# Performance work log

Hardware: AMD Instinct MI355X
Metric: run time of the kernel (lower is better)

## Reference

```python
import jax, jax.numpy as jnp
import numpy as np

N = 10000
E = 320000
DIN = 256
HID = 64
HEADS = 4
LAT = 32
NEG_SLOPE = 0.2


def _layer_params(key, din, heads, out_c):
    ks = jax.random.split(key, 6)
    s_in = 1.0 / np.sqrt(din)
    return dict(
        Wl=jax.random.normal(ks[0], (din, heads * out_c), jnp.float32) * s_in,
        bl=jnp.zeros((heads * out_c,), jnp.float32),
        Wr=jax.random.normal(ks[1], (din, heads * out_c), jnp.float32) * s_in,
        br=jnp.zeros((heads * out_c,), jnp.float32),
        att=jax.random.normal(ks[2], (heads, out_c), jnp.float32) * (1.0 / np.sqrt(out_c)),
        bo=jnp.zeros((heads * out_c,), jnp.float32),
    )


def setup_inputs() -> dict:
    key = jax.random.key(0)
    ks = jax.random.split(key, 8)
    inp = {
        "x": jax.random.normal(ks[0], (N, DIN), jnp.float32),
        "edge_index": jax.random.randint(ks[1], (2, E), 0, N, jnp.int64 if jax.config.jax_enable_x64 else jnp.int32),
        "eps": jax.random.normal(ks[2], (N, LAT), jnp.float32),
    }
    p0 = _layer_params(ks[3], DIN, HEADS, HID)
    p1 = _layer_params(ks[4], HID * HEADS, HEADS, HID)
    pmu = _layer_params(ks[5], HID * HEADS, 1, LAT)
    plv = _layer_params(ks[6], HID * HEADS, 1, LAT)
    for tag, p in (("l0", p0), ("l1", p1), ("mu", pmu), ("lv", plv)):
        for k, v in p.items():
            inp[f"{k}_{tag}"] = v
    return inp


def _gatv2(h, src, dst, Wl, bl, Wr, br, att, bo, heads, out_c, concat):
    # GATv2: e_ij = att . LeakyReLU(lin_l(x_j) + lin_r(x_i)), softmax over j for each i,
    # out_i = sum_j alpha_ij * lin_l(x_j). src = j (source), dst = i (target).
    xl = (h @ Wl + bl).reshape(-1, heads, out_c)  # [N,H,C]
    xr = (h @ Wr + br).reshape(-1, heads, out_c)
    e = jax.nn.leaky_relu(xl[src] + xr[dst], NEG_SLOPE)  # [E,H,C]
    score = jnp.einsum('ehc,hc->eh', e, att)             # [E,H]
    smax = jax.ops.segment_max(score, dst, num_segments=N)
    ex = jnp.exp(score - smax[dst])
    denom = jax.ops.segment_sum(ex, dst, num_segments=N)
    alpha = ex / (denom[dst] + 1e-16)                    # [E,H]
    out = jax.ops.segment_sum(alpha[:, :, None] * xl[src], dst, num_segments=N)  # [N,H,C]
    out = out.reshape(N, heads * out_c) if concat else out.mean(axis=1)
    return out + bo


def reference(x, edge_index, eps,
              Wl_l0, bl_l0, Wr_l0, br_l0, att_l0, bo_l0,
              Wl_l1, bl_l1, Wr_l1, br_l1, att_l1, bo_l1,
              Wl_mu, bl_mu, Wr_mu, br_mu, att_mu, bo_mu,
              Wl_lv, bl_lv, Wr_lv, br_lv, att_lv, bo_lv):
    loop = jnp.arange(N, dtype=edge_index.dtype)
    src = jnp.concatenate([edge_index[0], loop])  # add self-loops (PyG default)
    dst = jnp.concatenate([edge_index[1], loop])
    h = jax.nn.elu(_gatv2(x, src, dst, Wl_l0, bl_l0, Wr_l0, br_l0, att_l0, bo_l0, HEADS, HID, True))
    h = jax.nn.elu(_gatv2(h, src, dst, Wl_l1, bl_l1, Wr_l1, br_l1, att_l1, bo_l1, HEADS, HID, True))
    mu = _gatv2(h, src, dst, Wl_mu, bl_mu, Wr_mu, br_mu, att_mu, bo_mu, 1, LAT, False)
    log_var = _gatv2(h, src, dst, Wl_lv, bl_lv, Wr_lv, br_lv, att_lv, bo_lv, 1, LAT, False)
    z = mu + eps * jnp.exp(0.5 * log_var)  # reparameterize (training mode)
    adj_recon = z @ z.T                    # [N,N] dense decode
    return (adj_recon, mu, log_var)
```

## Files before the change

### kernel.cpp

```cpp
#include <hip/hip_runtime.h>
#include <hip/hip_bf16.h>
#include <math.h>

constexpr int Nn  = 10000;
constexpr int Ed  = 320000;
constexpr int DIN = 256;
constexpr float NEG = 0.2f;

constexpr size_t OFF_XL  = 0;
constexpr size_t OFF_XR  = 2560000;
constexpr size_t OFF_H   = 5120000;
constexpr size_t OFF_XSL = 7680000;
constexpr size_t OFF_XSR = 8320000;
constexpr size_t OFF_WLC = 8960000;
constexpr size_t OFF_WRC = 8976384;
constexpr size_t OFF_BLC = 8992768;
constexpr size_t OFF_BRC = 8992832;
constexpr size_t OFF_ATT = 8992896;
constexpr size_t OFF_BOC = 8992960;
constexpr size_t OFF_INT = 9000000;
constexpr int I_DEG = 0;
constexpr int I_ROW = 16384;
constexpr int I_CUR = 32768;
constexpr int I_CSR = 49152;
static_assert(OFF_INT + (I_CSR + Ed + Nn + 4) / 1 < 100000000, "scratch fits in adj region");

__global__ void k_init_deg(int* deg, int n) {
    int i = blockIdx.x * blockDim.x + threadIdx.x;
    if (i < n) deg[i] = 1;
}

__global__ void k_count(const int* __restrict__ dst, int* deg, int e) {
    int i = blockIdx.x * blockDim.x + threadIdx.x;
    if (i < e) atomicAdd(&deg[dst[i]], 1);
}

__global__ void k_scan(const int* __restrict__ deg, int* row_ptr, int* cursor, int n) {
    __shared__ int sums[256];
    int t = threadIdx.x;
    int chunk = (n + 255) / 256;
    int start = t * chunk, end = min(start + chunk, n);
    int s = 0;
    for (int i = start; i < end; ++i) s += deg[i];
    sums[t] = s;
    __syncthreads();
    for (int off = 1; off < 256; off <<= 1) {
        int v = (t >= off) ? sums[t - off] : 0;
        __syncthreads();
        sums[t] += v;
        __syncthreads();
    }
    int run = sums[t] - s;
    for (int i = start; i < end; ++i) { row_ptr[i] = run; cursor[i] = run; run += deg[i]; }
    if (t == 255) row_ptr[n] = sums[255];
}

__global__ void k_scatter(const int* __restrict__ src, const int* __restrict__ dst,
                          int* cursor, int* csr, int e, int n) {
    int i = blockIdx.x * blockDim.x + threadIdx.x;
    if (i < e) {
        int d = dst[i];
        int pos = atomicAdd(&cursor[d], 1);
        csr[pos] = src[i];
    } else if (i < e + n) {
        int v = i - e;
        int pos = atomicAdd(&cursor[v], 1);
        csr[pos] = v;
    }
}

__global__ __launch_bounds__(256) void k_gemm(const float* __restrict__ A,
                                              const float* __restrict__ W,
                                              const float* __restrict__ bias,
                                              float* __restrict__ out,
                                              int M, int Ncols) {
    constexpr int K = 256;
    __shared__ float As[32][68];
    __shared__ float Ws[32][64];
    int tid = threadIdx.x;
    int tx = tid & 15, ty = tid >> 4;
    int m0 = blockIdx.x * 64, n0 = blockIdx.y * 64;
    float acc[4][4] = {};
    int am = tid >> 2, akb = (tid & 3) * 8;
    int wk = tid >> 3, wnb = (tid & 7) * 8;
    const bool arow_ok = (m0 + am) < M;
    const float* Aptr = A + (size_t)(m0 + am) * K + akb;
    const float* Wptr = W + (size_t)wk * Ncols + n0 + wnb;

    for (int k0 = 0; k0 < K; k0 += 32) {
        float4 a0 = {0, 0, 0, 0}, a1 = {0, 0, 0, 0};
        if (arow_ok) {
            a0 = *(const float4*)(Aptr + k0);
            a1 = *(const float4*)(Aptr + k0 + 4);
        }
        float4 w0 = *(const float4*)(Wptr + (size_t)k0 * Ncols);
        float4 w1 = *(const float4*)(Wptr + (size_t)k0 * Ncols + 4);
        __syncthreads();
        As[akb + 0][am] = a0.x; As[akb + 1][am] = a0.y; As[akb + 2][am] = a0.z; As[akb + 3][am] = a0.w;
        As[akb + 4][am] = a1.x; As[akb + 5][am] = a1.y; As[akb + 6][am] = a1.z; As[akb + 7][am] = a1.w;
        *(float4*)&Ws[wk][wnb] = w0;
        *(float4*)&Ws[wk][wnb + 4] = w1;
        __syncthreads();
        #pragma unroll
        for (int k = 0; k < 32; ++k) {
            float4 a = *(const float4*)&As[k][ty * 4];
            float4 b = *(const float4*)&Ws[k][tx * 4];
            float av[4] = {a.x, a.y, a.z, a.w};
            float bv[4] = {b.x, b.y, b.z, b.w};
            #pragma unroll
            for (int i2 = 0; i2 < 4; ++i2)
                #pragma unroll
                for (int j2 = 0; j2 < 4; ++j2)
                    acc[i2][j2] = fmaf(av[i2], bv[j2], acc[i2][j2]);
        }
    }
    #pragma unroll
    for (int i2 = 0; i2 < 4; ++i2) {
        int row = m0 + ty * 4 + i2;
        if (row < M) {
            int col = n0 + tx * 4;
            float4 o;
            o.x = acc[i2][0] + bias[col + 0];
            o.y = acc[i2][1] + bias[col + 1];
            o.z = acc[i2][2] + bias[col + 2];
            o.w = acc[i2][3] + bias[col + 3];
            *(float4*)&out[(size_t)row * Ncols + col] = o;
        }
    }
}

__device__ __forceinline__ float lrelu(float x) { return x > 0.f ? x : NEG * x; }

template <bool DO_ELU>
__global__ __launch_bounds__(256) void k_gat4(const float* __restrict__ xl,
                                              const float* __restrict__ xr,
                                              const float* __restrict__ att,
                                              const float* __restrict__ bo,
                                              const int* __restrict__ row_ptr,
                                              const int* __restrict__ csr,
                                              float* __restrict__ out, int n) {
    int lane = threadIdx.x & 63;
    int node = (blockIdx.x * blockDim.x + threadIdx.x) >> 6;
    if (node >= n) return;
    int f = lane * 4;
    float4 xrr  = *(const float4*)&xr[(size_t)node * 256 + f];
    float4 attr = *(const float4*)&att[f];
    float m = -INFINITY, d = 0.f;
    float4 acc = {0.f, 0.f, 0.f, 0.f};

    int e0 = row_ptr[node], e1 = row_ptr[node + 1];
    int e = e0;
    for (; e + 1 < e1; e += 2) {
        int ja = csr[e], jb = csr[e + 1];
        float4 va = *(const float4*)&xl[(size_t)ja * 256 + f];
        float4 vb = *(const float4*)&xl[(size_t)jb * 256 + f];
        float ta = attr.x * lrelu(va.x + xrr.x) + attr.y * lrelu(va.y + xrr.y)
                 + attr.z * lrelu(va.z + xrr.z) + attr.w * lrelu(va.w + xrr.w);
        float tb = attr.x * lrelu(vb.x + xrr.x) + attr.y * lrelu(vb.y + xrr.y)
                 + attr.z * lrelu(vb.z + xrr.z) + attr.w * lrelu(vb.w + xrr.w);
        #pragma unroll
        for (int mask = 1; mask <= 8; mask <<= 1) {
            ta += __shfl_xor(ta, mask, 64);
            tb += __shfl_xor(tb, mask, 64);
        }
        float mn = fmaxf(m, fmaxf(ta, tb));
        float sc = __expf(m - mn);
        float pa = __expf(ta - mn), pb = __expf(tb - mn);
        d = d * sc + pa + pb;
        acc.x = acc.x * sc + pa * va.x + pb * vb.x;
        acc.y = acc.y * sc + pa * va.y + pb * vb.y;
        acc.z = acc.z * sc + pa * va.z + pb * vb.z;
        acc.w = acc.w * sc + pa * va.w + pb * vb.w;
        m = mn;
    }
    if (e < e1) {
        int j = csr[e];
        float4 v = *(const float4*)&xl[(size_t)j * 256 + f];
        float t = attr.x * lrelu(v.x + xrr.x) + attr.y * lrelu(v.y + xrr.y)
                + attr.z * lrelu(v.z + xrr.z) + attr.w * lrelu(v.w + xrr.w);
        #pragma unroll
        for (int mask = 1; mask <= 8; mask <<= 1) t += __shfl_xor(t, mask, 64);
        float mn = fmaxf(m, t);
        float sc = __expf(m - mn), p = __expf(t - mn);
        d = d * sc + p;
        acc.x = acc.x * sc + p * v.x;
        acc.y = acc.y * sc + p * v.y;
        acc.z = acc.z * sc + p * v.z;
        acc.w = acc.w * sc + p * v.w;
        m = mn;
    }
    float inv = 1.f / (d + 1e-16f);
    float4 bo4 = *(const float4*)&bo[f];
    float4 o;
    o.x = acc.x * inv + bo4.x;
    o.y = acc.y * inv + bo4.y;
    o.z = acc.z * inv + bo4.z;
    o.w = acc.w * inv + bo4.w;
    if (DO_ELU) {
        o.x = o.x > 0.f ? o.x : expm1f(o.x);
        o.y = o.y > 0.f ? o.y : expm1f(o.y);
        o.z = o.z > 0.f ? o.z : expm1f(o.z);
        o.w = o.w > 0.f ? o.w : expm1f(o.w);
    }
    *(float4*)&out[(size_t)node * 256 + f] = o;
}

template <int H, int C, bool DO_ELU, bool SPLIT>
__global__ __launch_bounds__(256) void k_gat(const float* __restrict__ xl,
                                             const float* __restrict__ xr,
                                             const float* __restrict__ att,
                                             const float* __restrict__ bo,
                                             const int* __restrict__ row_ptr,
                                             const int* __restrict__ csr,
                                             float* __restrict__ out0,
                                             float* __restrict__ out1, int n) {
    constexpr int F = H * C;
    constexpr int R = F / 64;
    int lane = threadIdx.x & 63;
    int node = (blockIdx.x * blockDim.x + threadIdx.x) >> 6;
    if (node >= n) return;

    float xrr[R], attr[R], m[R], d[R], acc[R];
    #pragma unroll
    for (int r = 0; r < R; ++r) {
        xrr[r]  = xr[(size_t)node * F + r * 64 + lane];
        attr[r] = att[r * 64 + lane];
        m[r] = -INFINITY;
        d[r] = 0.f;
        acc[r] = 0.f;
    }
    int e0 = row_ptr[node], e1 = row_ptr[node + 1];
    for (int e = e0; e < e1; ++e) {
        int j = csr[e];
        float v[R], s[R];
        #pragma unroll
        for (int r = 0; r < R; ++r) {
            v[r] = xl[(size_t)j * F + r * 64 + lane];
            float t = v[r] + xrr[r];
            t = (t > 0.f) ? t : NEG * t;
            t *= attr[r];
            #pragma unroll
            for (int mask = C / 2; mask >= 1; mask >>= 1)
                t += __shfl_xor(t, mask, 64);
            s[r] = t;
        }
        #pragma unroll
        for (int r = 0; r < R; ++r) {
            if (s[r] > m[r]) {
                float sc = __expf(m[r] - s[r]);
                d[r] *= sc; acc[r] *= sc; m[r] = s[r];
            }
            float p = __expf(s[r] - m[r]);
            d[r] += p;
            acc[r] = fmaf(p, v[r], acc[r]);
        }
    }
    #pragma unroll
    for (int r = 0; r < R; ++r) {
        float o = acc[r] / (d[r] + 1e-16f) + bo[r * 64 + lane];
        if (DO_ELU) o = (o > 0.f) ? o : expm1f(o);
        if (SPLIT) {
            int f = r * 64 + lane;
            int h = f / C, c = f % C;
            float* op = (h == 0) ? out0 : out1;
            op[(size_t)node * C + c] = o;
        } else {
            out0[(size_t)node * F + r * 64 + lane] = o;
        }
    }
}

__global__ void k_cat(const float* __restrict__ Wlmu, const float* __restrict__ Wllv,
                      const float* __restrict__ Wrmu, const float* __restrict__ Wrlv,
                      const float* __restrict__ blmu, const float* __restrict__ bllv,
                      const float* __restrict__ brmu, const float* __restrict__ brlv,
                      const float* __restrict__ attmu, const float* __restrict__ attlv,
                      const float* __restrict__ bomu, const float* __restrict__ bolv,
                      float* WLC, float* WRC, float* BLC, float* BRC, float* ATTC, float* BOC) {
    int i = blockIdx.x * blockDim.x + threadIdx.x;
    if (i < 256 * 64) {
        int k = i >> 6, c = i & 63;
        WLC[i] = (c < 32) ? Wlmu[k * 32 + c] : Wllv[k * 32 + c - 32];
        WRC[i] = (c < 32) ? Wrmu[k * 32 + c] : Wrlv[k * 32 + c - 32];
    }
    if (i < 64) {
        BLC[i]  = (i < 32) ? blmu[i]  : bllv[i - 32];
        BRC[i]  = (i < 32) ? brmu[i]  : brlv[i - 32];
        ATTC[i] = (i < 32) ? attmu[i] : attlv[i - 32];
        BOC[i]  = (i < 32) ? bomu[i]  : bolv[i - 32];
    }
}

__device__ __forceinline__ unsigned short f2bf(float x) {
    unsigned int u = __float_as_uint(x);
    unsigned int r = (u + 0x7FFFu + ((u >> 16) & 1u)) >> 16;
    return (unsigned short)r;
}
__device__ __forceinline__ float bf2f(unsigned short b) {
    return __uint_as_float(((unsigned int)b) << 16);
}

__global__ void k_z2(const float* __restrict__ mu, const float* __restrict__ lv,
                     const float* __restrict__ eps,
                     unsigned short* __restrict__ zhi,
                     unsigned short* __restrict__ zlo, int n) {
    int i = blockIdx.x * blockDim.x + threadIdx.x;
    if (i < n * 8) {
        float4 m4 = ((const float4*)mu)[i];
        float4 l4 = ((const float4*)lv)[i];
        float4 e4 = ((const float4*)eps)[i];
        float zv[4];
        zv[0] = m4.x + e4.x * __expf(0.5f * l4.x);
        zv[1] = m4.y + e4.y * __expf(0.5f * l4.y);
        zv[2] = m4.z + e4.z * __expf(0.5f * l4.z);
        zv[3] = m4.w + e4.w * __expf(0.5f * l4.w);
        ushort4 h, lo;
        h.x = f2bf(zv[0]); lo.x = f2bf(zv[0] - bf2f(h.x));
        h.y = f2bf(zv[1]); lo.y = f2bf(zv[1] - bf2f(h.y));
        h.z = f2bf(zv[2]); lo.z = f2bf(zv[2] - bf2f(h.z));
        h.w = f2bf(zv[3]); lo.w = f2bf(zv[3] - bf2f(h.w));
        *(ushort4*)&zhi[(size_t)i * 4] = h;
        *(ushort4*)&zlo[(size_t)i * 4] = lo;
    }
}

typedef short bf16x8 __attribute__((ext_vector_type(8)));
typedef float f32x4  __attribute__((ext_vector_type(4)));
constexpr int JTM = 25;

__global__ __launch_bounds__(256) void k_adjm(const unsigned short* __restrict__ zhi,
                                              const unsigned short* __restrict__ zlo,
                                              float* __restrict__ adj, int n) {
    int wave  = threadIdx.x >> 6;
    int l     = threadIdx.x & 63;
    int strip = blockIdx.y * 4 + wave;
    if (strip * 16 >= n) return;
    int i0   = strip * 16;
    int arow = i0 + (l & 15);
    int koff = (l >> 4) * 8;
    bf16x8 a_hi = *(const bf16x8*)(zhi + (size_t)arow * 32 + koff);
    bf16x8 a_lo = *(const bf16x8*)(zlo + (size_t)arow * 32 + koff);
    int crow = i0 + (l >> 4) * 4;

    for (int t = 0; t < JTM; ++t) {
        int j0   = (blockIdx.x * JTM + t) * 16;
        int brow = j0 + (l & 15);
        bf16x8 b_hi = *(const bf16x8*)(zhi + (size_t)brow * 32 + koff);
        bf16x8 b_lo = *(const bf16x8*)(zlo + (size_t)brow * 32 + koff);
        f32x4 acc = {0.f, 0.f, 0.f, 0.f};
        acc = __builtin_amdgcn_mfma_f32_16x16x32_bf16(a_hi, b_hi, acc, 0, 0, 0);
        acc = __builtin_amdgcn_mfma_f32_16x16x32_bf16(a_hi, b_lo, acc, 0, 0, 0);
        acc = __builtin_amdgcn_mfma_f32_16x16x32_bf16(a_lo, b_hi, acc, 0, 0, 0);
        size_t base = (size_t)crow * n + j0 + (l & 15);
        adj[base]                 = acc[0];
        adj[base + (size_t)n]     = acc[1];
        adj[base + (size_t)n * 2] = acc[2];
        adj[base + (size_t)n * 3] = acc[3];
    }
}

constexpr int JT = 8;
__global__ __launch_bounds__(256) void k_adj_fb(const float* __restrict__ mu,
                                                const float* __restrict__ lv,
                                                const float* __restrict__ eps,
                                                float* __restrict__ adj, int n) {
    __shared__ float Zi[32][68];
    __shared__ float Zj[32][68];
    int tid = threadIdx.x;
    int tx = tid & 15, ty = tid >> 4;
    int i0 = blockIdx.y * 64;
    int r = tid >> 2, kq = (tid & 3) * 8;

    auto load8 = [&](int row, float4& a, float4& b) {
        a = make_float4(0.f, 0.f, 0.f, 0.f);
        b = make_float4(0.f, 0.f, 0.f, 0.f);
        if (row < n) {
            float4 m0 = *(const float4*)&mu[row * 32 + kq];
            float4 l0 = *(const float4*)&lv[row * 32 + kq];
            float4 e0 = *(const float4*)&eps[row * 32 + kq];
            float4 m1 = *(const float4*)&mu[row * 32 + kq + 4];
            float4 l1 = *(const float4*)&lv[row * 32 + kq + 4];
            float4 e1 = *(const float4*)&eps[row * 32 + kq + 4];
            a.x = m0.x + e0.x * __expf(0.5f * l0.x);
            a.y = m0.y + e0.y * __expf(0.5f * l0.y);
            a.z = m0.z + e0.z * __expf(0.5f * l0.z);
            a.w = m0.w + e0.w * __expf(0.5f * l0.w);
            b.x = m1.x + e1.x * __expf(0.5f * l1.x);
            b.y = m1.y + e1.y * __expf(0.5f * l1.y);
            b.z = m1.z + e1.z * __expf(0.5f * l1.z);
            b.w = m1.w + e1.w * __expf(0.5f * l1.w);
        }
    };

    {
        float4 a, b;
        load8(i0 + r, a, b);
        Zi[kq + 0][r] = a.x; Zi[kq + 1][r] = a.y; Zi[kq + 2][r] = a.z; Zi[kq + 3][r] = a.w;
        Zi[kq + 4][r] = b.x; Zi[kq + 5][r] = b.y; Zi[kq + 6][r] = b.z; Zi[kq + 7][r] = b.w;
    }
    __syncthreads();
    float4 af[32];
    #pragma unroll
    for (int k = 0; k < 32; ++k) af[k] = *(const float4*)&Zi[k][ty * 4];

    for (int jt = 0; jt < JT; ++jt) {
        int j0 = (blockIdx.x * JT + jt) * 64;
        if (j0 >= n) break;
        {
            float4 a, b;
            load8(j0 + r, a, b);
            __syncthreads();
            Zj[kq + 0][r] = a.x; Zj[kq + 1][r] = a.y; Zj[kq + 2][r] = a.z; Zj[kq + 3][r] = a.w;
            Zj[kq + 4][r] = b.x; Zj[kq + 5][r] = b.y; Zj[kq + 6][r] = b.z; Zj[kq + 7][r] = b.w;
            __syncthreads();
        }
        float acc[4][4] = {};
        #pragma unroll
        for (int k = 0; k < 32; ++k) {
            float4 b = *(const float4*)&Zj[k][tx * 4];
            float av[4] = {af[k].x, af[k].y, af[k].z, af[k].w};
            float bv[4] = {b.x, b.y, b.z, b.w};
            #pragma unroll
            for (int i2 = 0; i2 < 4; ++i2)
                #pragma unroll
                for (int j2 = 0; j2 < 4; ++j2)
                    acc[i2][j2] = fmaf(av[i2], bv[j2], acc[i2][j2]);
        }
        int col = j0 + tx * 4;
        if (col < n) {
            #pragma unroll
            for (int i2 = 0; i2 < 4; ++i2) {
                int row = i0 + ty * 4 + i2;
                if (row < n) {
                    float4 o = {acc[i2][0], acc[i2][1], acc[i2][2], acc[i2][3]};
                    *(float4*)&adj[(size_t)row * n + col] = o;
                }
            }
        }
    }
}

extern "C" void kernel_launch(void* const* d_in, const int* in_sizes, int n_in,
                              void* d_out, int out_size, void* d_ws, size_t ws_size,
                              hipStream_t stream) {
    const float* x      = (const float*)d_in[0];
    const int*   edges  = (const int*)d_in[1];
    const float* eps    = (const float*)d_in[2];
    const float* Wl0 = (const float*)d_in[3];
    const float* bl0 = (const float*)d_in[4];
    const float* Wr0 = (const float*)d_in[5];
    const float* br0 = (const float*)d_in[6];
    const float* at0 = (const float*)d_in[7];
    const float* bo0 = (const float*)d_in[8];
    const float* Wl1 = (const float*)d_in[9];
    const float* bl1 = (const float*)d_in[10];
    const float* Wr1 = (const float*)d_in[11];
    const float* br1 = (const float*)d_in[12];
    const float* at1 = (const float*)d_in[13];
    const float* bo1 = (const float*)d_in[14];
    const float* Wlmu = (const float*)d_in[15];
    const float* blmu = (const float*)d_in[16];
    const float* Wrmu = (const float*)d_in[17];
    const float* brmu = (const float*)d_in[18];
    const float* atmu = (const float*)d_in[19];
    const float* bomu = (const float*)d_in[20];
    const float* Wllv = (const float*)d_in[21];
    const float* bllv = (const float*)d_in[22];
    const float* Wrlv = (const float*)d_in[23];
    const float* brlv = (const float*)d_in[24];
    const float* atlv = (const float*)d_in[25];
    const float* bolv = (const float*)d_in[26];

    float* base   = (float*)d_out;
    float* adj    = base;
    float* mu_out = base + (size_t)Nn * Nn;
    float* lv_out = mu_out + (size_t)Nn * 32;

    float* XL  = base + OFF_XL;
    float* XR  = base + OFF_XR;
    float* H   = base + OFF_H;
    float* XSL = base + OFF_XSL;
    float* XSR = base + OFF_XSR;
    float* WLC = base + OFF_WLC;
    float* WRC = base + OFF_WRC;
    float* BLC = base + OFF_BLC;
    float* BRC = base + OFF_BRC;
    float* ATT = base + OFF_ATT;
    float* BOC = base + OFF_BOC;
    int* ib  = (int*)(base + OFF_INT);
    int* deg = ib + I_DEG;
    int* row = ib + I_ROW;
    int* cur = ib + I_CUR;
    int* csr = ib + I_CSR;
    const int* srcp = edges;
    const int* dstp = edges + Ed;

    k_init_deg<<<(Nn + 255) / 256, 256, 0, stream>>>(deg, Nn);
    k_count<<<(Ed + 255) / 256, 256, 0, stream>>>(dstp, deg, Ed);
    k_scan<<<1, 256, 0, stream>>>(deg, row, cur, Nn);
    k_scatter<<<(Ed + Nn + 255) / 256, 256, 0, stream>>>(srcp, dstp, cur, csr, Ed, Nn);

    dim3 g4(157, 4), g1(157, 1);
    k_gemm<<<g4, 256, 0, stream>>>(x, Wl0, bl0, XL, Nn, 256);
    k_gemm<<<g4, 256, 0, stream>>>(x, Wr0, br0, XR, Nn, 256);
    k_gat4<true><<<2500, 256, 0, stream>>>(XL, XR, at0, bo0, row, csr, H, Nn);
    k_gemm<<<g4, 256, 0, stream>>>(H, Wl1, bl1, XL, Nn, 256);
    k_gemm<<<g4, 256, 0, stream>>>(H, Wr1, br1, XR, Nn, 256);
    k_gat4<true><<<2500, 256, 0, stream>>>(XL, XR, at1, bo1, row, csr, H, Nn);
    k_cat<<<64, 256, 0, stream>>>(Wlmu, Wllv, Wrmu, Wrlv, blmu, bllv, brmu, brlv,
                                  atmu, atlv, bomu, bolv, WLC, WRC, BLC, BRC, ATT, BOC);
    k_gemm<<<g1, 256, 0, stream>>>(H, WLC, BLC, XSL, Nn, 64);
    k_gemm<<<g1, 256, 0, stream>>>(H, WRC, BRC, XSR, Nn, 64);
    k_gat<2, 32, false, true><<<2500, 256, 0, stream>>>(XSL, XSR, ATT, BOC, row, csr, mu_out, lv_out, Nn);

    size_t need = (size_t)Nn * 32 * 2 * sizeof(unsigned short);
    if (ws_size >= need) {
        unsigned short* zhi = (unsigned short*)d_ws;
        unsigned short* zlo = zhi + (size_t)Nn * 32;
        k_z2<<<(Nn * 8 + 255) / 256, 256, 0, stream>>>(mu_out, lv_out, eps, zhi, zlo, Nn);
        dim3 ga(25, 157);
        k_adjm<<<ga, 256, 0, stream>>>(zhi, zlo, adj, Nn);
    } else {
        dim3 ga(20, 157);
        k_adj_fb<<<ga, 256, 0, stream>>>(mu_out, lv_out, eps, adj, Nn);
    }
}
```

Measured before the change: 447.4 us.

## Replace FP32 SIMT GEMMs with split-bf16 MFMA GEMMs fusing left/right projections

Replaces the shared-memory FP32 FMA GEMM with an MFMA kernel that runs bf16 hi/lo split products (three MFMAs per k-step) to keep close to FP32 accuracy. Activations are converted to hi/lo bf16 by a new conversion kernel before each layer, and weights are transposed and split once per call. The lin_l and lin_r projections now share one launch that reuses the A fragments held in registers. This trades extra conversion kernels and weight traffic read straight from global memory, with no LDS staging, for matrix-core throughput.

```diff
diff --git a/kernel.cpp b/kernel.cpp
--- a/kernel.cpp
+++ b/kernel.cpp
@@ -7,23 +7,31 @@
 constexpr int DIN = 256;
 constexpr float NEG = 0.2f;
 
-constexpr size_t OFF_XL  = 0;
-constexpr size_t OFF_XR  = 2560000;
-constexpr size_t OFF_H   = 5120000;
-constexpr size_t OFF_XSL = 7680000;
-constexpr size_t OFF_XSR = 8320000;
-constexpr size_t OFF_WLC = 8960000;
-constexpr size_t OFF_WRC = 8976384;
-constexpr size_t OFF_BLC = 8992768;
-constexpr size_t OFF_BRC = 8992832;
-constexpr size_t OFF_ATT = 8992896;
-constexpr size_t OFF_BOC = 8992960;
-constexpr size_t OFF_INT = 9000000;
+constexpr size_t OFF_XL   = 0;
+constexpr size_t OFF_XR   = 2560000;
+constexpr size_t OFF_H    = 5120000;
+constexpr size_t OFF_XSL  = 7680000;
+constexpr size_t OFF_XSR  = 8320000;
+constexpr size_t OFF_AH   = 8960000;
+constexpr size_t OFF_AL   = 10240000;
+constexpr size_t OFF_WT0LH = 11520000, OFF_WT0LL = 11552768;
+constexpr size_t OFF_WT0RH = 11585536, OFF_WT0RL = 11618304;
+constexpr size_t OFF_WT1LH = 11651072, OFF_WT1LL = 11683840;
+constexpr size_t OFF_WT1RH = 11716608, OFF_WT1RL = 11749376;
+constexpr size_t OFF_WTCLH = 11782144, OFF_WTCLL = 11790336;
+constexpr size_t OFF_WTCRH = 11798528, OFF_WTCRL = 11806720;
+constexpr size_t OFF_WLC  = 11814912;
+constexpr size_t OFF_WRC  = 11831296;
+constexpr size_t OFF_BLC  = 11847680;
+constexpr size_t OFF_BRC  = 11847744;
+constexpr size_t OFF_ATT  = 11847808;
+constexpr size_t OFF_BOC  = 11847872;
+constexpr size_t OFF_INT  = 12000000;
 constexpr int I_DEG = 0;
 constexpr int I_ROW = 16384;
 constexpr int I_CUR = 32768;
 constexpr int I_CSR = 49152;
-static_assert(OFF_INT + (I_CSR + Ed + Nn + 4) / 1 < 100000000, "scratch fits in adj region");
+static_assert(OFF_INT + (I_CSR + Ed + Nn + 4) < 100000000, "scratch fits in adj region");
 
 __global__ void k_init_deg(int* deg, int n) {
     int i = blockIdx.x * blockDim.x + threadIdx.x;
@@ -69,62 +77,95 @@
     }
 }
 
-__global__ __launch_bounds__(256) void k_gemm(const float* __restrict__ A,
-                                              const float* __restrict__ W,
-                                              const float* __restrict__ bias,
-                                              float* __restrict__ out,
-                                              int M, int Ncols) {
-    constexpr int K = 256;
-    __shared__ float As[32][68];
-    __shared__ float Ws[32][64];
-    int tid = threadIdx.x;
-    int tx = tid & 15, ty = tid >> 4;
-    int m0 = blockIdx.x * 64, n0 = blockIdx.y * 64;
-    float acc[4][4] = {};
-    int am = tid >> 2, akb = (tid & 3) * 8;
-    int wk = tid >> 3, wnb = (tid & 7) * 8;
-    const bool arow_ok = (m0 + am) < M;
-    const float* Aptr = A + (size_t)(m0 + am) * K + akb;
-    const float* Wptr = W + (size_t)wk * Ncols + n0 + wnb;
-
-    for (int k0 = 0; k0 < K; k0 += 32) {
-        float4 a0 = {0, 0, 0, 0}, a1 = {0, 0, 0, 0};
-        if (arow_ok) {
-            a0 = *(const float4*)(Aptr + k0);
-            a1 = *(const float4*)(Aptr + k0 + 4);
-        }
-        float4 w0 = *(const float4*)(Wptr + (size_t)k0 * Ncols);
-        float4 w1 = *(const float4*)(Wptr + (size_t)k0 * Ncols + 4);
-        __syncthreads();
-        As[akb + 0][am] = a0.x; As[akb + 1][am] = a0.y; As[akb + 2][am] = a0.z; As[akb + 3][am] = a0.w;
-        As[akb + 4][am] = a1.x; As[akb + 5][am] = a1.y; As[akb + 6][am] = a1.z; As[akb + 7][am] = a1.w;
-        *(float4*)&Ws[wk][wnb] = w0;
-        *(float4*)&Ws[wk][wnb + 4] = w1;
-        __syncthreads();
-        #pragma unroll
-        for (int k = 0; k < 32; ++k) {
-            float4 a = *(const float4*)&As[k][ty * 4];
-            float4 b = *(const float4*)&Ws[k][tx * 4];
-            float av[4] = {a.x, a.y, a.z, a.w};
-            float bv[4] = {b.x, b.y, b.z, b.w};
+__device__ __forceinline__ unsigned short f2bf(float x) {
+    unsigned int u = __float_as_uint(x);
+    unsigned int r = (u + 0x7FFFu + ((u >> 16) & 1u)) >> 16;
+    return (unsigned short)r;
+}
+__device__ __forceinline__ float bf2f(unsigned short b) {
+    return __uint_as_float(((unsigned int)b) << 16);
+}
+
+typedef short bf16x8 __attribute__((ext_vector_type(8)));
+typedef float f32x4  __attribute__((ext_vector_type(4)));
+
+__global__ void k_conv(const float* __restrict__ A, unsigned short* __restrict__ ahi,
+                       unsigned short* __restrict__ alo, int total4) {
+    int i = blockIdx.x * blockDim.x + threadIdx.x;
+    if (i < total4) {
+        float4 v = ((const float4*)A)[i];
+        ushort4 h, lo;
+        h.x = f2bf(v.x); lo.x = f2bf(v.x - bf2f(h.x));
+        h.y = f2bf(v.y); lo.y = f2bf(v.y - bf2f(h.y));
+        h.z = f2bf(v.z); lo.z = f2bf(v.z - bf2f(h.z));
+        h.w = f2bf(v.w); lo.w = f2bf(v.w - bf2f(h.w));
+        ((ushort4*)ahi)[i] = h;
+        ((ushort4*)alo)[i] = lo;
+    }
+}
+
+__global__ void k_wt(const float* __restrict__ W, unsigned short* __restrict__ wthi,
+                     unsigned short* __restrict__ wtlo, int Nc) {
+    int i = blockIdx.x * blockDim.x + threadIdx.x;
+    if (i < Nc * 256) {
+        int nrow = i >> 8, k = i & 255;
+        float w = W[k * Nc + nrow];
+        unsigned short h = f2bf(w);
+        wthi[i] = h;
+        wtlo[i] = f2bf(w - bf2f(h));
+    }
+}
+
+template <int NC>
+__global__ __launch_bounds__(256) void k_gemm_bf(
+        const unsigned short* __restrict__ ah, const unsigned short* __restrict__ al,
+        const unsigned short* __restrict__ wLh, const unsigned short* __restrict__ wLl,
+        const unsigned short* __restrict__ wRh, const unsigned short* __restrict__ wRl,
+        const float* __restrict__ biasL, const float* __restrict__ biasR,
+        float* __restrict__ outL, float* __restrict__ outR, int n) {
+    int wave = threadIdx.x >> 6;
+    int l    = threadIdx.x & 63;
+    int strip = blockIdx.x * 4 + wave;
+    if (strip * 16 >= n) return;
+    int i0   = strip * 16;
+    int arow = i0 + (l & 15);
+    int koff = (l >> 4) * 8;
+    bf16x8 a_hi[8], a_lo[8];
+    #pragma unroll
+    for (int kk = 0; kk < 8; ++kk) {
+        a_hi[kk] = *(const bf16x8*)(ah + (size_t)arow * 256 + kk * 32 + koff);
+        a_lo[kk] = *(const bf16x8*)(al + (size_t)arow * 256 + kk * 32 + koff);
+    }
+    int crow = i0 + (l >> 4) * 4;
+    int ncol = l & 15;
+
+    const unsigned short* wh[2] = {wLh, wRh};
+    const unsigned short* wl[2] = {wLl, wRl};
+    const float* bias[2] = {biasL, biasR};
+    float* outp[2] = {outL, outR};
+
+    #pragma unroll
+    for (int s = 0; s < 2; ++s) {
+        for (int jt = 0; jt < NC / 16; ++jt) {
+            int jc = jt * 16 + ncol;
+            const unsigned short* bh = wh[s] + (size_t)jc * 256 + koff;
+            const unsigned short* bo = wl[s] + (size_t)jc * 256 + koff;
+            f32x4 acc = {0.f, 0.f, 0.f, 0.f};
             #pragma unroll
-            for (int i2 = 0; i2 < 4; ++i2)
-                #pragma unroll
-                for (int j2 = 0; j2 < 4; ++j2)
-                    acc[i2][j2] = fmaf(av[i2], bv[j2], acc[i2][j2]);
-        }
-    }
-    #pragma unroll
-    for (int i2 = 0; i2 < 4; ++i2) {
-        int row = m0 + ty * 4 + i2;
-        if (row < M) {
-            int col = n0 + tx * 4;
-            float4 o;
-            o.x = acc[i2][0] + bias[col + 0];
-            o.y = acc[i2][1] + bias[col + 1];
-            o.z = acc[i2][2] + bias[col + 2];
-            o.w = acc[i2][3] + bias[col + 3];
-            *(float4*)&out[(size_t)row * Ncols + col] = o;
+            for (int kk = 0; kk < 8; ++kk) {
+                bf16x8 b_h = *(const bf16x8*)(bh + kk * 32);
+                bf16x8 b_l = *(const bf16x8*)(bo + kk * 32);
+                acc = __builtin_amdgcn_mfma_f32_16x16x32_bf16(a_hi[kk], b_h, acc, 0, 0, 0);
+                acc = __builtin_amdgcn_mfma_f32_16x16x32_bf16(a_hi[kk], b_l, acc, 0, 0, 0);
+                acc = __builtin_amdgcn_mfma_f32_16x16x32_bf16(a_lo[kk], b_h, acc, 0, 0, 0);
+            }
+            float bv = bias[s][jc];
+            float* op = outp[s];
+            size_t ob = (size_t)crow * NC + jc;
+            op[ob]              = acc[0] + bv;
+            op[ob + NC]         = acc[1] + bv;
+            op[ob + (size_t)NC * 2] = acc[2] + bv;
+            op[ob + (size_t)NC * 3] = acc[3] + bv;
         }
     }
 }
@@ -291,15 +332,6 @@
     }
 }
 
-__device__ __forceinline__ unsigned short f2bf(float x) {
-    unsigned int u = __float_as_uint(x);
-    unsigned int r = (u + 0x7FFFu + ((u >> 16) & 1u)) >> 16;
-    return (unsigned short)r;
-}
-__device__ __forceinline__ float bf2f(unsigned short b) {
-    return __uint_as_float(((unsigned int)b) << 16);
-}
-
 __global__ void k_z2(const float* __restrict__ mu, const float* __restrict__ lv,
                      const float* __restrict__ eps,
                      unsigned short* __restrict__ zhi,
@@ -324,8 +356,6 @@
     }
 }
 
-typedef short bf16x8 __attribute__((ext_vector_type(8)));
-typedef float f32x4  __attribute__((ext_vector_type(4)));
 constexpr int JTM = 25;
 
 __global__ __launch_bounds__(256) void k_adjm(const unsigned short* __restrict__ zhi,
@@ -481,6 +511,20 @@
     float* H   = base + OFF_H;
     float* XSL = base + OFF_XSL;
     float* XSR = base + OFF_XSR;
+    unsigned short* AH = (unsigned short*)(base + OFF_AH);
+    unsigned short* AL = (unsigned short*)(base + OFF_AL);
+    unsigned short* WT0LH = (unsigned short*)(base + OFF_WT0LH);
+    unsigned short* WT0LL = (unsigned short*)(base + OFF_WT0LL);
+    unsigned short* WT0RH = (unsigned short*)(base + OFF_WT0RH);
+    unsigned short* WT0RL = (unsigned short*)(base + OFF_WT0RL);
+    unsigned short* WT1LH = (unsigned short*)(base + OFF_WT1LH);
+    unsigned short* WT1LL = (unsigned short*)(base + OFF_WT1LL);
+    unsigned short* WT1RH = (unsigned short*)(base + OFF_WT1RH);
+    unsigned short* WT1RL = (unsigned short*)(base + OFF_WT1RL);
+    unsigned short* WTCLH = (unsigned short*)(base + OFF_WTCLH);
+    unsigned short* WTCLL = (unsigned short*)(base + OFF_WTCLL);
+    unsigned short* WTCRH = (unsigned short*)(base + OFF_WTCRH);
+    unsigned short* WTCRL = (unsigned short*)(base + OFF_WTCRL);
     float* WLC = base + OFF_WLC;
     float* WRC = base + OFF_WRC;
     float* BLC = base + OFF_BLC;
@@ -500,17 +544,27 @@
     k_scan<<<1, 256, 0, stream>>>(deg, row, cur, Nn);
     k_scatter<<<(Ed + Nn + 255) / 256, 256, 0, stream>>>(srcp, dstp, cur, csr, Ed, Nn);
 
-    dim3 g4(157, 4), g1(157, 1);
-    k_gemm<<<g4, 256, 0, stream>>>(x, Wl0, bl0, XL, Nn, 256);
-    k_gemm<<<g4, 256, 0, stream>>>(x, Wr0, br0, XR, Nn, 256);
-    k_gat4<true><<<2500, 256, 0, stream>>>(XL, XR, at0, bo0, row, csr, H, Nn);
-    k_gemm<<<g4, 256, 0, stream>>>(H, Wl1, bl1, XL, Nn, 256);
-    k_gemm<<<g4, 256, 0, stream>>>(H, Wr1, br1, XR, Nn, 256);
-    k_gat4<true><<<2500, 256, 0, stream>>>(XL, XR, at1, bo1, row, csr, H, Nn);
     k_cat<<<64, 256, 0, stream>>>(Wlmu, Wllv, Wrmu, Wrlv, blmu, bllv, brmu, brlv,
                                   atmu, atlv, bomu, bolv, WLC, WRC, BLC, BRC, ATT, BOC);
-    k_gemm<<<g1, 256, 0, stream>>>(H, WLC, BLC, XSL, Nn, 64);
-    k_gemm<<<g1, 256, 0, stream>>>(H, WRC, BRC, XSR, Nn, 64);
+    k_wt<<<256, 256, 0, stream>>>(Wl0, WT0LH, WT0LL, 256);
+    k_wt<<<256, 256, 0, stream>>>(Wr0, WT0RH, WT0RL, 256);
+    k_wt<<<256, 256, 0, stream>>>(Wl1, WT1LH, WT1LL, 256);
+    k_wt<<<256, 256, 0, stream>>>(Wr1, WT1RH, WT1RL, 256);
+    k_wt<<<64, 256, 0, stream>>>(WLC, WTCLH, WTCLL, 64);
+    k_wt<<<64, 256, 0, stream>>>(WRC, WTCRH, WTCRL, 64);
+
+    constexpr int CONV_BLKS = (Nn * 256 / 4 + 255) / 256;
+    k_conv<<<CONV_BLKS, 256, 0, stream>>>(x, AH, AL, Nn * 256 / 4);
+    k_gemm_bf<256><<<157, 256, 0, stream>>>(AH, AL, WT0LH, WT0LL, WT0RH, WT0RL,
+                                            bl0, br0, XL, XR, Nn);
+    k_gat4<true><<<2500, 256, 0, stream>>>(XL, XR, at0, bo0, row, csr, H, Nn);
+    k_conv<<<CONV_BLKS, 256, 0, stream>>>(H, AH, AL, Nn * 256 / 4);
+    k_gemm_bf<256><<<157, 256, 0, stream>>>(AH, AL, WT1LH, WT1LL, WT1RH, WT1RL,
+                                            bl1, br1, XL, XR, Nn);
+    k_gat4<true><<<2500, 256, 0, stream>>>(XL, XR, at1, bo1, row, csr, H, Nn);
+    k_conv<<<CONV_BLKS, 256, 0, stream>>>(H, AH, AL, Nn * 256 / 4);
+    k_gemm_bf<64><<<157, 256, 0, stream>>>(AH, AL, WTCLH, WTCLL, WTCRH, WTCRL,
+                                           BLC, BRC, XSL, XSR, Nn);
     k_gat<2, 32, false, true><<<2500, 256, 0, stream>>>(XSL, XSR, ATT, BOC, row, csr, mu_out, lv_out, Nn);
 
     size_t need = (size_t)Nn * 32 * 2 * sizeof(unsigned short);
```

Measured after the change: 503.3 us. 1.12x slower.
